# Performance work log

Hardware: AMD Instinct MI355X
Metric: run time of the kernel (lower is better)

## Reference

```python
import jax, jax.numpy as jnp
import numpy as np

NUM_FREQS = 10
NUM_VOXELS = 512
N_POINTS = 262144
IN_DIM = 3
INPUT_CH = IN_DIM + 2 * NUM_FREQS * IN_DIM  # 63


def posenc(x, num_freqs):
    # NeRF positional encoding: [x, sin(x*2^0), cos(x*2^0), ..., sin(x*2^(F-1)), cos(x*2^(F-1))]
    freqs = (2.0 ** jnp.arange(num_freqs)).astype(x.dtype)           # (F,)
    xf = x[:, None, :] * freqs[None, :, None]                        # (N, F, D)
    sc = jnp.stack([jnp.sin(xf), jnp.cos(xf)], axis=2)               # (N, F, 2, D)
    return jnp.concatenate([x, sc.reshape(x.shape[0], -1)], axis=-1)  # (N, D + 2*F*D)


def setup_inputs() -> dict:
    key = jax.random.key(0)
    k_x, k_w, k_v = jax.random.split(key, 3)
    X = jax.random.normal(k_x, (N_POINTS, IN_DIM), dtype=jnp.float32)
    # linear_mappings reshaped to (3*num_voxels, input_ch), used as Linear weight (no bias)
    W = jax.random.normal(k_w, (3 * NUM_VOXELS, INPUT_CH), dtype=jnp.float32) * 0.02
    row_ids = jnp.arange(N_POINTS, dtype=jnp.int64 if jax.config.jax_enable_x64 else jnp.int32)
    voxel_ids = jax.random.randint(k_v, (N_POINTS,), 0, NUM_VOXELS)
    return {"X": X, "W": W, "row_ids": row_ids, "voxel_ids": voxel_ids}


def reference(X, W, row_ids, voxel_ids):
    encoded_X = posenc(X, NUM_FREQS)                      # (N, 63)
    rgb_clusters = encoded_X @ W.T                        # (N, 3*num_voxels) -- wasteful dense GEMM
    # col_indices per selected row: [3v, 3v+1, 3v+2]
    cols = jnp.stack([3 * voxel_ids, 3 * voxel_ids + 1, 3 * voxel_ids + 2], axis=1)  # (M, 3)
    vals = rgb_clusters[row_ids[:, None], cols]           # (M, 3)
    rgb = jnp.zeros((X.shape[0], 3), dtype=X.dtype)
    rgb = rgb.at[row_ids].set(vals)
    return rgb
```

## Files before the change

### kernel.cpp

```cpp
#include <hip/hip_runtime.h>
#include <math.h>

#define N_POINTS   262144
#define NUM_FREQS  10
#define NUM_VOXELS 512

__device__ __forceinline__ unsigned short f2bf(float f) {
    unsigned int u = __float_as_uint(f);
    unsigned int r = (u + 0x7fffu + ((u >> 16) & 1u)) >> 16;
    return (unsigned short)r;
}
__device__ __forceinline__ float bf_lo(unsigned int u) {
    return __uint_as_float(u << 16);
}
__device__ __forceinline__ float bf_hi(unsigned int u) {
    return __uint_as_float(u & 0xffff0000u);
}

__global__ __launch_bounds__(192) void pack_w(
    const float* __restrict__ W, unsigned short* __restrict__ Wp)
{
    const int v = blockIdx.x;
    const int t = threadIdx.x;
    if (t < 189) {
        const int row = t / 63, col = t % 63;
        Wp[v * 192 + row * 64 + col] = f2bf(W[v * 189 + t]);
    } else {
        Wp[v * 192 + (t - 189) * 64 + 63] = 0;
    }
}

__global__ __launch_bounds__(256) void voxlin_main(
    const float* __restrict__ X,
    const unsigned short* __restrict__ Wp,
    const int* __restrict__ row_ids,
    const int* __restrict__ voxel_ids,
    float* __restrict__ out)
{
    const int i = blockIdx.x * 256 + threadIdx.x;
    if (i >= N_POINTS) return;

    const float x0 = X[3*i + 0];
    const float x1 = X[3*i + 1];
    const float x2 = X[3*i + 2];
    const int   v  = voxel_ids[i];

    float enc[64];
    enc[0] = x0; enc[1] = x1; enc[2] = x2;
    enc[63] = 0.0f;

    float s0, c0, s1, c1, s2, c2;
    sincosf(x0, &s0, &c0);
    sincosf(x1, &s1, &c1);
    sincosf(x2, &s2, &c2);
    #pragma unroll
    for (int f = 0; f < NUM_FREQS; ++f) {
        const int b = 3 + 6*f;
        enc[b+0] = s0; enc[b+1] = s1; enc[b+2] = s2;
        enc[b+3] = c0; enc[b+4] = c1; enc[b+5] = c2;
        if (f < NUM_FREQS - 1) {
            const float ns0 = 2.0f*s0*c0, nc0 = c0*c0 - s0*s0;
            const float ns1 = 2.0f*s1*c1, nc1 = c1*c1 - s1*s1;
            const float ns2 = 2.0f*s2*c2, nc2 = c2*c2 - s2*s2;
            s0 = ns0; c0 = nc0; s1 = ns1; c1 = nc1; s2 = ns2; c2 = nc2;
        }
    }

    const uint4* __restrict__ wb = (const uint4*)(Wp + (size_t)v * 192);
    float acc[3];
    #pragma unroll
    for (int r = 0; r < 3; ++r) {
        float a = 0.0f;
        #pragma unroll
        for (int k = 0; k < 8; ++k) {
            const uint4 q = wb[r * 8 + k];
            const int e = 8 * k;
            a += bf_lo(q.x) * enc[e+0] + bf_hi(q.x) * enc[e+1]
               + bf_lo(q.y) * enc[e+2] + bf_hi(q.y) * enc[e+3]
               + bf_lo(q.z) * enc[e+4] + bf_hi(q.z) * enc[e+5]
               + bf_lo(q.w) * enc[e+6] + bf_hi(q.w) * enc[e+7];
        }
        acc[r] = a;
    }

    const int rr = row_ids[i];
    out[3*rr + 0] = acc[0];
    out[3*rr + 1] = acc[1];
    out[3*rr + 2] = acc[2];
}

__global__ __launch_bounds__(256) void voxlin_fallback(
    const float* __restrict__ X, const float* __restrict__ W,
    const int* __restrict__ row_ids, const int* __restrict__ voxel_ids,
    float* __restrict__ out)
{
    const int i = blockIdx.x * 256 + threadIdx.x;
    if (i >= N_POINTS) return;
    const float x0 = X[3*i], x1 = X[3*i+1], x2 = X[3*i+2];
    const int v = voxel_ids[i];
    const float* __restrict__ w0 = W + v * 189;
    const float* __restrict__ w1 = w0 + 63;
    const float* __restrict__ w2 = w0 + 126;

    float a0 = x0*w0[0] + x1*w0[1] + x2*w0[2];
    float a1 = x0*w1[0] + x1*w1[1] + x2*w1[2];
    float a2 = x0*w2[0] + x1*w2[1] + x2*w2[2];
    float s0, c0, s1, c1, s2, c2;
    sincosf(x0, &s0, &c0); sincosf(x1, &s1, &c1); sincosf(x2, &s2, &c2);
    #pragma unroll
    for (int f = 0; f < NUM_FREQS; ++f) {
        const int b = 3 + 6*f;
        a0 += s0*w0[b] + s1*w0[b+1] + s2*w0[b+2] + c0*w0[b+3] + c1*w0[b+4] + c2*w0[b+5];
        a1 += s0*w1[b] + s1*w1[b+1] + s2*w1[b+2] + c0*w1[b+3] + c1*w1[b+4] + c2*w1[b+5];
        a2 += s0*w2[b] + s1*w2[b+1] + s2*w2[b+2] + c0*w2[b+3] + c1*w2[b+4] + c2*w2[b+5];
        if (f < NUM_FREQS - 1) {
            const float ns0 = 2.0f*s0*c0, nc0 = c0*c0 - s0*s0;
            const float ns1 = 2.0f*s1*c1, nc1 = c1*c1 - s1*s1;
            const float ns2 = 2.0f*s2*c2, nc2 = c2*c2 - s2*s2;
            s0 = ns0; c0 = nc0; s1 = ns1; c1 = nc1; s2 = ns2; c2 = nc2;
        }
    }
    const int r = row_ids[i];
    out[3*r] = a0; out[3*r+1] = a1; out[3*r+2] = a2;
}

extern "C" void kernel_launch(void* const* d_in, const int* in_sizes, int n_in,
                              void* d_out, int out_size, void* d_ws, size_t ws_size,
                              hipStream_t stream) {
    const float* X         = (const float*)d_in[0];
    const float* W         = (const float*)d_in[1];
    const int*   row_ids   = (const int*)d_in[2];
    const int*   voxel_ids = (const int*)d_in[3];
    float*       out       = (float*)d_out;

    const int grid256 = (N_POINTS + 255) / 256;
    const size_t need = (size_t)NUM_VOXELS * 192 * sizeof(unsigned short);

    if (ws_size >= need) {
        unsigned short* Wp = (unsigned short*)d_ws;
        pack_w<<<NUM_VOXELS, 192, 0, stream>>>(W, Wp);
        voxlin_main<<<grid256, 256, 0, stream>>>(X, Wp, row_ids, voxel_ids, out);
    } else {
        voxlin_fallback<<<grid256, 256, 0, stream>>>(X, W, row_ids, voxel_ids, out);
    }
}
```

Before: 80.73 us.

## Sort points by voxel within each block before posenc dot product

Replaces the per-point kernel with a 1024-thread block that builds a shared-memory histogram and prefix scan over voxel ids, then reorders points so neighbouring threads share voxel weight rows. This aims to improve weight-load coherence and cache reuse. It adds atomics, a multi-step scan with many barriers and large blocks with reduced occupancy, and output writes become scattered.

```diff
diff --git a/kernel.cpp b/kernel.cpp
--- a/kernel.cpp
+++ b/kernel.cpp
@@ -7,15 +7,10 @@
 
 __device__ __forceinline__ unsigned short f2bf(float f) {
     unsigned int u = __float_as_uint(f);
-    unsigned int r = (u + 0x7fffu + ((u >> 16) & 1u)) >> 16;
-    return (unsigned short)r;
+    return (unsigned short)((u + 0x7fffu + ((u >> 16) & 1u)) >> 16);
 }
-__device__ __forceinline__ float bf_lo(unsigned int u) {
-    return __uint_as_float(u << 16);
-}
-__device__ __forceinline__ float bf_hi(unsigned int u) {
-    return __uint_as_float(u & 0xffff0000u);
-}
+__device__ __forceinline__ float bf_lo(unsigned int u) { return __uint_as_float(u << 16); }
+__device__ __forceinline__ float bf_hi(unsigned int u) { return __uint_as_float(u & 0xffff0000u); }
 
 __global__ __launch_bounds__(192) void pack_w(
     const float* __restrict__ W, unsigned short* __restrict__ Wp)
@@ -30,21 +25,10 @@
     }
 }
 
-__global__ __launch_bounds__(256) void voxlin_main(
-    const float* __restrict__ X,
-    const unsigned short* __restrict__ Wp,
-    const int* __restrict__ row_ids,
-    const int* __restrict__ voxel_ids,
-    float* __restrict__ out)
+__device__ __forceinline__ void posenc_pack_dot(
+    float x0, float x1, float x2, const unsigned short* __restrict__ Wp, int v,
+    float& a0, float& a1, float& a2)
 {
-    const int i = blockIdx.x * 256 + threadIdx.x;
-    if (i >= N_POINTS) return;
-
-    const float x0 = X[3*i + 0];
-    const float x1 = X[3*i + 1];
-    const float x2 = X[3*i + 2];
-    const int   v  = voxel_ids[i];
-
     float enc[64];
     enc[0] = x0; enc[1] = x1; enc[2] = x2;
     enc[63] = 0.0f;
@@ -82,11 +66,62 @@
         }
         acc[r] = a;
     }
+    a0 = acc[0]; a1 = acc[1]; a2 = acc[2];
+}
 
-    const int rr = row_ids[i];
-    out[3*rr + 0] = acc[0];
-    out[3*rr + 1] = acc[1];
-    out[3*rr + 2] = acc[2];
+__global__ __launch_bounds__(1024, 1) void voxlin_sorted(
+    const float* __restrict__ X,
+    const unsigned short* __restrict__ Wp,
+    const int* __restrict__ row_ids,
+    const int* __restrict__ voxel_ids,
+    float* __restrict__ out)
+{
+    __shared__ float4 pts[1024];
+    __shared__ int    meta[1024];
+    __shared__ int    hist[NUM_VOXELS];
+    __shared__ int    cur[NUM_VOXELS];
+
+    const int t = threadIdx.x;
+    const int i = blockIdx.x * 1024 + t;
+
+    const int   v  = voxel_ids[i];
+    const float x0 = X[3*i + 0];
+    const float x1 = X[3*i + 1];
+    const float x2 = X[3*i + 2];
+    const int   r  = row_ids[i];
+
+    if (t < NUM_VOXELS) hist[t] = 0;
+    __syncthreads();
+    atomicAdd(&hist[v], 1);
+    __syncthreads();
+
+    const int c = (t < NUM_VOXELS) ? hist[t] : 0;
+    #pragma unroll
+    for (int off = 1; off < NUM_VOXELS; off <<= 1) {
+        int add = (t < NUM_VOXELS && t >= off) ? hist[t - off] : 0;
+        __syncthreads();
+        if (t < NUM_VOXELS) hist[t] += add;
+        __syncthreads();
+    }
+    if (t < NUM_VOXELS) cur[t] = hist[t] - c;
+    __syncthreads();
+
+    const int pos = atomicAdd(&cur[v], 1);
+    pts[pos]  = make_float4(x0, x1, x2, 0.0f);
+    meta[pos] = r | (v << 18);
+    __syncthreads();
+
+    const float4 q = pts[t];
+    const int    m = meta[t];
+    const int    sv = m >> 18;
+    const int    sr = m & 0x3FFFF;
+
+    float a0, a1, a2;
+    posenc_pack_dot(q.x, q.y, q.z, Wp, sv, a0, a1, a2);
+
+    out[3*sr + 0] = a0;
+    out[3*sr + 1] = a1;
+    out[3*sr + 2] = a2;
 }
 
 __global__ __launch_bounds__(256) void voxlin_fallback(
@@ -120,8 +155,8 @@
             s0 = ns0; c0 = nc0; s1 = ns1; c1 = nc1; s2 = ns2; c2 = nc2;
         }
     }
-    const int r = row_ids[i];
-    out[3*r] = a0; out[3*r+1] = a1; out[3*r+2] = a2;
+    const int rr = row_ids[i];
+    out[3*rr] = a0; out[3*rr+1] = a1; out[3*rr+2] = a2;
 }
 
 extern "C" void kernel_launch(void* const* d_in, const int* in_sizes, int n_in,
@@ -133,14 +168,13 @@
     const int*   voxel_ids = (const int*)d_in[3];
     float*       out       = (float*)d_out;
 
-    const int grid256 = (N_POINTS + 255) / 256;
     const size_t need = (size_t)NUM_VOXELS * 192 * sizeof(unsigned short);
 
     if (ws_size >= need) {
         unsigned short* Wp = (unsigned short*)d_ws;
         pack_w<<<NUM_VOXELS, 192, 0, stream>>>(W, Wp);
-        voxlin_main<<<grid256, 256, 0, stream>>>(X, Wp, row_ids, voxel_ids, out);
+        voxlin_sorted<<<N_POINTS / 1024, 1024, 0, stream>>>(X, Wp, row_ids, voxel_ids, out);
     } else {
-        voxlin_fallback<<<grid256, 256, 0, stream>>>(X, W, row_ids, voxel_ids, out);
+        voxlin_fallback<<<(N_POINTS + 255) / 256, 256, 0, stream>>>(X, W, row_ids, voxel_ids, out);
     }
 }
```

Result: faster. 76.23 us (-5.6%).

## Quantize weights to int8 per-row and stage whole table in LDS

Applied to the files above, without the earlier changes.

Weights are quantized to int8 with a per-row absmax scale, so the full 512-voxel table fits in about 104 KB of shared memory. Each 1024-thread block copies the table into LDS, computes the encoding, then gathers its voxel's weights from LDS instead of global/L2. The aim is to remove scattered global gathers of weight rows. In exchange each block repeats a 104 KB load, occupancy is limited by LDS, and int8 quantization adds accuracy error beyond the previous bf16.

```diff
diff --git a/kernel.cpp b/kernel.cpp
--- a/kernel.cpp
+++ b/kernel.cpp
@@ -4,51 +4,69 @@
 #define N_POINTS   262144
 #define NUM_FREQS  10
 #define NUM_VOXELS 512
+#define VOX_U      13
+#define TAB_U      (NUM_VOXELS * VOX_U)
 
-__device__ __forceinline__ unsigned short f2bf(float f) {
-    unsigned int u = __float_as_uint(f);
-    unsigned int r = (u + 0x7fffu + ((u >> 16) & 1u)) >> 16;
-    return (unsigned short)r;
-}
-__device__ __forceinline__ float bf_lo(unsigned int u) {
-    return __uint_as_float(u << 16);
-}
-__device__ __forceinline__ float bf_hi(unsigned int u) {
-    return __uint_as_float(u & 0xffff0000u);
+
+__device__ __forceinline__ float sb(unsigned u, int b) {
+    return (float)((int)(u << (24 - 8 * b)) >> 24);
 }
 
-__global__ __launch_bounds__(192) void pack_w(
-    const float* __restrict__ W, unsigned short* __restrict__ Wp)
-{
-    const int v = blockIdx.x;
-    const int t = threadIdx.x;
-    if (t < 189) {
-        const int row = t / 63, col = t % 63;
-        Wp[v * 192 + row * 64 + col] = f2bf(W[v * 189 + t]);
-    } else {
-        Wp[v * 192 + (t - 189) * 64 + 63] = 0;
-    }
+__device__ __forceinline__ float dot16(uint4 q, const float* e) {
+    float s;
+    s  = sb(q.x,0)*e[ 0] + sb(q.x,1)*e[ 1] + sb(q.x,2)*e[ 2] + sb(q.x,3)*e[ 3];
+    s += sb(q.y,0)*e[ 4] + sb(q.y,1)*e[ 5] + sb(q.y,2)*e[ 6] + sb(q.y,3)*e[ 7];
+    s += sb(q.z,0)*e[ 8] + sb(q.z,1)*e[ 9] + sb(q.z,2)*e[10] + sb(q.z,3)*e[11];
+    s += sb(q.w,0)*e[12] + sb(q.w,1)*e[13] + sb(q.w,2)*e[14] + sb(q.w,3)*e[15];
+    return s;
 }
 
-__global__ __launch_bounds__(256) void voxlin_main(
+__global__ __launch_bounds__(192) void pack_w_q8(
+    const float* __restrict__ W, char* __restrict__ Wq)
+{
+    const int v   = blockIdx.x;
+    const int t   = threadIdx.x;
+    const int row = t >> 6, col = t & 63;
+    const float w = (col < 63) ? W[v*189 + row*63 + col] : 0.0f;
+
+    float m = fabsf(w);
+    #pragma unroll
+    for (int d = 32; d > 0; d >>= 1) m = fmaxf(m, __shfl_xor(m, d));
+
+    const float scale = m * (1.0f / 127.0f);
+    const float inv   = (m > 0.0f) ? 127.0f / m : 0.0f;
+    int q = __float2int_rn(w * inv);
+    q = max(-127, min(127, q));
+    Wq[v*208 + row*64 + col] = (char)q;
+    if (col == 0) ((float*)(Wq + v*208 + 192))[row] = scale;
+}
+
+__global__ __launch_bounds__(1024, 4) void voxlin_lds(
     const float* __restrict__ X,
-    const unsigned short* __restrict__ Wp,
+    const uint4* __restrict__ Wq,
     const int* __restrict__ row_ids,
     const int* __restrict__ voxel_ids,
     float* __restrict__ out)
 {
-    const int i = blockIdx.x * 256 + threadIdx.x;
-    if (i >= N_POINTS) return;
+    __shared__ uint4 table[TAB_U];
 
+    const int t = threadIdx.x;
+    #pragma unroll
+    for (int u = 0; u < 7; ++u) {
+        const int idx = t + u * 1024;
+        if (idx < TAB_U) table[idx] = Wq[idx];
+    }
+
+    const int   i  = blockIdx.x * 1024 + t;
     const float x0 = X[3*i + 0];
     const float x1 = X[3*i + 1];
     const float x2 = X[3*i + 2];
     const int   v  = voxel_ids[i];
+    const int   r  = row_ids[i];
 
     float enc[64];
     enc[0] = x0; enc[1] = x1; enc[2] = x2;
     enc[63] = 0.0f;
-
     float s0, c0, s1, c1, s2, c2;
     sincosf(x0, &s0, &c0);
     sincosf(x1, &s1, &c1);
@@ -66,27 +84,29 @@
         }
     }
 
-    const uint4* __restrict__ wb = (const uint4*)(Wp + (size_t)v * 192);
+    __syncthreads();
+
+    const int base = v * VOX_U;
+    const uint4 su = table[base + 12];
+    const float sc0 = __uint_as_float(su.x);
+    const float sc1 = __uint_as_float(su.y);
+    const float sc2 = __uint_as_float(su.z);
+
     float acc[3];
     #pragma unroll
-    for (int r = 0; r < 3; ++r) {
-        float a = 0.0f;
-        #pragma unroll
-        for (int k = 0; k < 8; ++k) {
-            const uint4 q = wb[r * 8 + k];
-            const int e = 8 * k;
-            a += bf_lo(q.x) * enc[e+0] + bf_hi(q.x) * enc[e+1]
-               + bf_lo(q.y) * enc[e+2] + bf_hi(q.y) * enc[e+3]
-               + bf_lo(q.z) * enc[e+4] + bf_hi(q.z) * enc[e+5]
-               + bf_lo(q.w) * enc[e+6] + bf_hi(q.w) * enc[e+7];
-        }
-        acc[r] = a;
+    for (int rr = 0; rr < 3; ++rr) {
+        const uint4 q0 = table[base + rr*4 + 0];
+        const uint4 q1 = table[base + rr*4 + 1];
+        const uint4 q2 = table[base + rr*4 + 2];
+        const uint4 q3 = table[base + rr*4 + 3];
+        float s = dot16(q0, enc +  0) + dot16(q1, enc + 16)
+                + dot16(q2, enc + 32) + dot16(q3, enc + 48);
+        acc[rr] = s;
     }
 
-    const int rr = row_ids[i];
-    out[3*rr + 0] = acc[0];
-    out[3*rr + 1] = acc[1];
-    out[3*rr + 2] = acc[2];
+    out[3*r + 0] = acc[0] * sc0;
+    out[3*r + 1] = acc[1] * sc1;
+    out[3*r + 2] = acc[2] * sc2;
 }
 
 __global__ __launch_bounds__(256) void voxlin_fallback(
@@ -101,7 +121,6 @@
     const float* __restrict__ w0 = W + v * 189;
     const float* __restrict__ w1 = w0 + 63;
     const float* __restrict__ w2 = w0 + 126;
-
     float a0 = x0*w0[0] + x1*w0[1] + x2*w0[2];
     float a1 = x0*w1[0] + x1*w1[1] + x2*w1[2];
     float a2 = x0*w2[0] + x1*w2[1] + x2*w2[2];
@@ -120,8 +139,8 @@
             s0 = ns0; c0 = nc0; s1 = ns1; c1 = nc1; s2 = ns2; c2 = nc2;
         }
     }
-    const int r = row_ids[i];
-    out[3*r] = a0; out[3*r+1] = a1; out[3*r+2] = a2;
+    const int rr = row_ids[i];
+    out[3*rr] = a0; out[3*rr+1] = a1; out[3*rr+2] = a2;
 }
 
 extern "C" void kernel_launch(void* const* d_in, const int* in_sizes, int n_in,
@@ -133,14 +152,14 @@
     const int*   voxel_ids = (const int*)d_in[3];
     float*       out       = (float*)d_out;
 
-    const int grid256 = (N_POINTS + 255) / 256;
-    const size_t need = (size_t)NUM_VOXELS * 192 * sizeof(unsigned short);
+    const size_t need = (size_t)TAB_U * 16;
 
     if (ws_size >= need) {
-        unsigned short* Wp = (unsigned short*)d_ws;
-        pack_w<<<NUM_VOXELS, 192, 0, stream>>>(W, Wp);
-        voxlin_main<<<grid256, 256, 0, stream>>>(X, Wp, row_ids, voxel_ids, out);
+        char* Wq = (char*)d_ws;
+        pack_w_q8<<<NUM_VOXELS, 192, 0, stream>>>(W, Wq);
+        voxlin_lds<<<N_POINTS / 1024, 1024, 0, stream>>>(
+            X, (const uint4*)Wq, row_ids, voxel_ids, out);
     } else {
-        voxlin_fallback<<<grid256, 256, 0, stream>>>(X, W, row_ids, voxel_ids, out);
+        voxlin_fallback<<<(N_POINTS + 255) / 256, 256, 0, stream>>>(X, W, row_ids, voxel_ids, out);
     }
 }
```

Result: slower. 87.67 us (+8.6%).
